# Kernel optimization log

Hardware: AMD Instinct MI355X
Metric: run time of the kernel (lower is better)

## Reference

```python
import jax, jax.numpy as jnp
import numpy as np

D, B, T, d = 4, 512, 64, 256  # num_dof, batch, seq_length, per-dof state dim


def setup_inputs() -> dict:
    key = jax.random.key(0)
    ks = jax.random.split(key, 17)
    w = lambda k, s: jax.random.normal(k, s, dtype=jnp.float32) * 0.05
    return {
        "x": jax.random.normal(ks[0], (D, B, T, d), dtype=jnp.float32),
        "wu": w(ks[1], (D, 2 * d, d)), "wf": w(ks[2], (D, 2 * d, d)),
        "wo": w(ks[3], (D, 2 * d, d)), "wc": w(ks[4], (D, 2 * d, d)),
        "bu": w(ks[5], (D, d)), "bf": w(ks[6], (D, d)),
        "bo": w(ks[7], (D, d)), "bc": w(ks[8], (D, d)),
        "gwu": w(ks[9], (D, D * d, d)), "gwf": w(ks[10], (D, D * d, d)),
        "gwo": w(ks[11], (D, D * d, d)), "gwc": w(ks[12], (D, D * d, d)),
        "gbu": w(ks[13], (D, d)), "gbf": w(ks[14], (D, d)),
        "gbo": w(ks[15], (D, d)), "gbc": w(ks[16], (D, d)),
    }


def reference(x, wu, wf, wo, wc, bu, bf, bo, bc,
              gwu, gwf, gwo, gwc, gbu, gbf, gbo, gbc):
    # x: [D, B, T, d]  (dof-stacked inputs_list)
    nD, nB, nT, nd = x.shape
    h0 = jnp.zeros((nD, nB, nd), x.dtype)
    m0 = jnp.zeros((nD, nB, nd), x.dtype)
    xt = jnp.transpose(x, (2, 0, 1, 3))  # [T, D, B, d]

    def step(carry, x_t):
        h, m = carry  # each [D, B, d]
        # --- per-dof LSTM cell (dofs independent here) ---
        inp = jnp.concatenate([x_t, h], axis=-1)  # [D, B, 2d]
        gu = jax.nn.sigmoid(jnp.einsum('dbi,dij->dbj', inp, wu) + bu[:, None, :])
        gf = jax.nn.sigmoid(jnp.einsum('dbi,dij->dbj', inp, wf) + bf[:, None, :])
        go = jax.nn.sigmoid(jnp.einsum('dbi,dij->dbj', inp, wo) + bo[:, None, :])
        gc = jnp.tanh(jnp.einsum('dbi,dij->dbj', inp, wc) + bc[:, None, :])
        m = gf * m + gu * gc
        h = jnp.tanh(go * m)
        # --- grid coupling step: hgrid = concat over dofs ---
        hg = jnp.transpose(h, (1, 0, 2)).reshape(nB, nD * nd)  # [B, D*d]
        gu2 = jax.nn.sigmoid(jnp.einsum('bs,dsj->dbj', hg, gwu) + gbu[:, None, :])
        gf2 = jax.nn.sigmoid(jnp.einsum('bs,dsj->dbj', hg, gwf) + gbf[:, None, :])
        go2 = jax.nn.sigmoid(jnp.einsum('bs,dsj->dbj', hg, gwo) + gbo[:, None, :])
        gc2 = jnp.tanh(jnp.einsum('bs,dsj->dbj', hg, gwc) + gbc[:, None, :])
        m = gf2 * m + gu2 * gc2
        h = jnp.tanh(go2 * m)
        return (h, m), None

    (h, m), _ = jax.lax.scan(step, (h0, m0), xt)
    # stacked [2, D, B, d]: [0]=h_list, [1]=m_list (dof along axis 1)
    return jnp.stack([h, m])
```

## Files before the change

kernel.cpp:

```cpp
#include <hip/hip_runtime.h>
#include <math.h>

#define NDOF 4
#define NB   512
#define NT   64
#define ND   256
#define NS   1024

#define GRID 256

typedef __attribute__((ext_vector_type(8))) __bf16 bf16x8;
typedef __attribute__((ext_vector_type(4))) float  f32x4;

__device__ __forceinline__ void gll16(const void* g, void* l) {
    __builtin_amdgcn_global_load_lds(
        (const __attribute__((address_space(1))) unsigned int*)g,
        (__attribute__((address_space(3))) unsigned int*)l, 16, 0, 0);
}

__device__ __forceinline__ float sig_(float x) { return 1.0f / (1.0f + __expf(-x)); }
__device__ __forceinline__ float tanh_(float x) {
    float e = __expf(-2.0f * fabsf(x));
    float t = (1.0f - e) / (1.0f + e);
    return copysignf(t, x);
}

__device__ __forceinline__ void store16_dev(__bf16* p, bf16x8 v) {
    asm volatile("global_store_dwordx4 %0, %1, off sc0 sc1" :: "v"(p), "v"(v) : "memory");
}

__device__ __forceinline__ void waitv0() {
    asm volatile("s_waitcnt vmcnt(0)" ::: "memory");
    __builtin_amdgcn_sched_barrier(0);
}
__device__ __forceinline__ void waitv8() {
    asm volatile("s_waitcnt vmcnt(8)" ::: "memory");
    __builtin_amdgcn_sched_barrier(0);
}
__device__ __forceinline__ void waitv12() {
    asm volatile("s_waitcnt vmcnt(12)" ::: "memory");
    __builtin_amdgcn_sched_barrier(0);
}

__device__ __forceinline__ void block_bar() {
    __builtin_amdgcn_sched_barrier(0);
    asm volatile("s_waitcnt lgkmcnt(0)\n\ts_barrier" ::: "memory");
    __builtin_amdgcn_sched_barrier(0);
}

__device__ __forceinline__ unsigned gen_load(const unsigned* p) {
    unsigned v;
    asm volatile("global_load_dword %0, %1, off sc0 sc1\n\ts_waitcnt vmcnt(0)"
                 : "=v"(v) : "v"(p) : "memory");
    return v;
}

struct __align__(64) Bar { unsigned cnt; unsigned gen; unsigned pad[14]; };

__device__ __forceinline__ void arrive_only(Bar* b, unsigned n, unsigned e) {
    unsigned prev = __hip_atomic_fetch_add(&b->cnt, 1u, __ATOMIC_RELAXED, __HIP_MEMORY_SCOPE_AGENT);
    if (prev == e * n - 1u)
        __hip_atomic_fetch_add(&b->gen, 1u, __ATOMIC_RELAXED, __HIP_MEMORY_SCOPE_AGENT);
}
__device__ __forceinline__ void poll_only(Bar* b, unsigned e) {
    unsigned spins = 0;
    while (gen_load(&b->gen) < e) {
        __builtin_amdgcn_s_sleep(1);
        if (++spins > (1u << 17)) break;
    }
}

struct Params {
    const __bf16* xbf;
    const __bf16* wT1;
    const __bf16* wT2;
    const float *b1u, *b1f, *b1o, *b1c;
    const float *b2u, *b2f, *b2o, *b2c;
    const __bf16* hInit;
    __bf16* ring;
    float*  out;
    Bar*    bars;
};

__device__ __forceinline__ void issueB(bf16x8* smem, const __bf16* wrow,
                                       int pair, int rot, int mask, int tid) {
    const int rowB = tid & 127;
    const int kgb  = (tid >> 7) & 1;
    const int bb = 2048 + (pair & 3) * 1024;
    const int k0 = ((pair + rot) & mask) * 64;
    #pragma unroll
    for (int i = 0; i < 4; ++i) {
        const int kg = kgb + 2 * i;
        gll16(wrow + k0 + kg * 8, &smem[bb + kg * 128 + rowB]);
    }
}
template<int XIT>
__device__ __forceinline__ void issueA(bf16x8* smem, const __bf16* ax,
                                       const __bf16* ah, int pair, int rot, int mask,
                                       int tid) {
    const int rowA = tid & 63;
    const int kga  = tid >> 6;
    const int bb = (pair & 3) * 512;
    const __bf16* base;
    if (XIT > 0 && pair < XIT) base = ax + (size_t)rowA * ND + pair * 64;
    else base = ah + (size_t)rowA * NS + (((pair + rot) & mask) * 64 - XIT * 64);
    #pragma unroll
    for (int i = 0; i < 2; ++i) {
        const int kg = kga + 4 * i;
        gll16(base + kg * 8, &smem[bb + kg * 64 + rowA]);
    }
}

template<int NIT, int XIT>
__device__ __forceinline__ void gemm_seg(bf16x8* smem,
    const __bf16* ax, const __bf16* ah, const __bf16* wrow, int rot,
    Bar* gateBar, unsigned gateE,
    f32x4 (&acc)[2][4], int lane, int wr, int ws, int tid)
{
    constexpr int NSEG = NIT / 2;
    #pragma unroll 1
    for (int s = 0; s < NSEG; ++s) {
        waitv0();
        block_bar();
        if (s == 1 && gateBar != nullptr) {
            if (tid == 0) poll_only(gateBar, gateE);
            block_bar();
        }
        if (s + 1 < NSEG) {
            issueB(smem, wrow, 2 * s + 2, rot, NIT - 1, tid);
            issueB(smem, wrow, 2 * s + 3, rot, NIT - 1, tid);
            issueA<XIT>(smem, ax, ah, 2 * s + 2, rot, NIT - 1, tid);
            issueA<XIT>(smem, ax, ah, 2 * s + 3, rot, NIT - 1, tid);
        }
        #pragma unroll
        for (int q = 0; q < 2; ++q) {
            const int bbA = ((2 * s + q) & 3) * 512;
            const int bbB = 2048 + ((2 * s + q) & 3) * 1024;
            #pragma unroll
            for (int sub = 0; sub < 2; ++sub) {
                const int kq = sub * 4 + (lane >> 4);
                bf16x8 a[2], b[4];
                #pragma unroll
                for (int mI = 0; mI < 2; ++mI)
                    a[mI] = smem[bbA + kq * 64 + wr + mI * 16 + (lane & 15)];
                #pragma unroll
                for (int g = 0; g < 4; ++g)
                    b[g] = smem[bbB + kq * 128 + g * 32 + ws * 16 + (lane & 15)];
                #pragma unroll
                for (int mI = 0; mI < 2; ++mI)
                    #pragma unroll
                    for (int g = 0; g < 4; ++g)
                        acc[mI][g] = __builtin_amdgcn_mfma_f32_16x16x32_bf16(a[mI], b[g], acc[mI][g], 0, 0, 0);
            }
        }
    }
}

__device__ __forceinline__ void epi_stage(const f32x4 (&acc)[2][4], float (&m_reg)[8],
    float bu, float bf_, float bo, float bc,
    char* stg, int wrL, int colq)
{
    #pragma unroll
    for (int mI = 0; mI < 2; ++mI) {
        #pragma unroll
        for (int r = 0; r < 4; ++r) {
            const int rowL = wrL + mI * 16 + r;
            const float gu = sig_(acc[mI][0][r] + bu);
            const float gf = sig_(acc[mI][1][r] + bf_);
            const float go = sig_(acc[mI][2][r] + bo);
            const float gc = tanh_(acc[mI][3][r] + bc);
            float& m = m_reg[mI * 4 + r];
            m = gf * m + gu * gc;
            ((__bf16*)(stg + rowL * 80))[colq] = (__bf16)tanh_(go * m);
        }
    }
}

__device__ __forceinline__ void flush_h(char* stg, __bf16* hbase, int r0,
                                        int scolBase, int tid)
{
    const int rowL = tid >> 2;
    const int off  = tid & 3;
    bf16x8 v = *(bf16x8*)(stg + rowL * 80 + off * 16);
    store16_dev(hbase + (size_t)(r0 + rowL) * NS + scolBase + off * 8, v);
}

__device__ __forceinline__ void epi_last(const f32x4 (&acc)[2][4], float (&m_reg)[8],
    float bu, float bf_, float bo, float bc,
    char* hs, char* ms, int wrL, int colq)
{
    #pragma unroll
    for (int mI = 0; mI < 2; ++mI) {
        #pragma unroll
        for (int r = 0; r < 4; ++r) {
            const int rowL = wrL + mI * 16 + r;
            const float gu = sig_(acc[mI][0][r] + bu);
            const float gf = sig_(acc[mI][1][r] + bf_);
            const float go = sig_(acc[mI][2][r] + bo);
            const float gc = tanh_(acc[mI][3][r] + bc);
            float& m = m_reg[mI * 4 + r];
            m = gf * m + gu * gc;
            ((float*)(hs + rowL * 144))[colq] = tanh_(go * m);
            ((float*)(ms + rowL * 144))[colq] = m;
        }
    }
}

__global__ __launch_bounds__(256, 1)
void lstm_persistent(Params p)
{
    __shared__ bf16x8 smem[6464];
    char* stg = (char*)&smem[6144];

    const int tid  = threadIdx.x;
    const int lane = tid & 63;
    const int wv   = tid >> 6;
    const int wr   = (wv >> 1) * 32;
    const int ws   = wv & 1;

    const int xcd   = blockIdx.x & 7;
    const int local = blockIdx.x >> 3;
    const int dof   = xcd & 3;
    const int rt    = (xcd >> 2) * 4 + (local >> 3);
    const int c0    = (local & 7) * 32;
    const int r0    = rt * 64;
    const int grp   = rt * 4 + dof;

    const int colq = ws * 16 + (lane & 15);
    const int scol = dof * ND + c0 + colq;
    const int scolBase = dof * ND + c0;
    const int wrL  = wr + (lane >> 4) * 4;

    const int rowB = tid & 127;
    const int npT  = dof * 1024 + (rowB >> 5) * 256 + c0 + (rowB & 31);
    const __bf16* wrow1 = p.wT1 + (size_t)npT * 512;
    const __bf16* wrow2 = p.wT2 + (size_t)npT * 1024;

    const float b1u = p.b1u[scol], b1f = p.b1f[scol], b1o = p.b1o[scol], b1c = p.b1c[scol];
    const float b2u = p.b2u[scol], b2f = p.b2f[scol], b2o = p.b2o[scol], b2c = p.b2c[scol];

    float m_reg[8];
    #pragma unroll
    for (int i = 0; i < 8; ++i) m_reg[i] = 0.f;

    Bar* bar32A = &p.bars[rt];
    Bar* bar8A  = &p.bars[8 + grp];
    Bar* bar8B  = &p.bars[40 + grp];
    const int rot2 = dof * 4;

    auto slot = [&](int i) -> __bf16* { return p.ring + ((size_t)i << 19); };

    {
        const __bf16* ax0 = p.xbf + ((size_t)(dof * NT) * NB + r0) * ND;
        issueB(smem, wrow1, 0, 0, 7, tid);
        issueB(smem, wrow1, 1, 0, 7, tid);
        issueA<4>(smem, ax0, nullptr, 0, 0, 7, tid);
        issueA<4>(smem, ax0, nullptr, 1, 0, 7, tid);
    }

    #pragma unroll 1
    for (int t = 0; t < NT; ++t) {
        const __bf16* ax  = p.xbf + ((size_t)(dof * NT + t) * NB + r0) * ND;
        const __bf16* ah1 = (t == 0 ? p.hInit : slot(2 * t - 1)) + (size_t)r0 * NS + dof * ND;
        __bf16* h1out = slot(2 * t);
        const __bf16* ah2 = slot(2 * t) + (size_t)r0 * NS;
        __bf16* h2out = slot(2 * t + 1);

        f32x4 acc[2][4];
        #pragma unroll
        for (int mI = 0; mI < 2; ++mI)
            #pragma unroll
            for (int g = 0; g < 4; ++g) acc[mI][g] = (f32x4){0.f, 0.f, 0.f, 0.f};

        gemm_seg<8, 4>(smem, ax, ah1, wrow1, 0, bar8B, (unsigned)t,
                       acc, lane, wr, ws, tid);

        epi_stage(acc, m_reg, b1u, b1f, b1o, b1c, stg, wrL, colq);
        block_bar();
        flush_h(stg, h1out, r0, scolBase, tid);
        issueB(smem, wrow2, 0, rot2, 15, tid);
        issueB(smem, wrow2, 1, rot2, 15, tid);
        waitv8();
        block_bar();
        if (tid == 0) {
            arrive_only(bar8A, 8, (unsigned)(t + 1));
            arrive_only(bar32A, 32, (unsigned)(t + 1));
            poll_only(bar8A, (unsigned)(t + 1));
        }
        block_bar();
        issueA<0>(smem, nullptr, ah2, 0, rot2, 15, tid);
        issueA<0>(smem, nullptr, ah2, 1, rot2, 15, tid);

        #pragma unroll
        for (int mI = 0; mI < 2; ++mI)
            #pragma unroll
            for (int g = 0; g < 4; ++g) acc[mI][g] = (f32x4){0.f, 0.f, 0.f, 0.f};

        gemm_seg<16, 0>(smem, nullptr, ah2, wrow2, rot2, bar32A, (unsigned)(t + 1),
                        acc, lane, wr, ws, tid);

        if (t + 1 < NT) {
            epi_stage(acc, m_reg, b2u, b2f, b2o, b2c, stg, wrL, colq);
            block_bar();
            flush_h(stg, h2out, r0, scolBase, tid);
            const __bf16* axn = p.xbf + ((size_t)(dof * NT + t + 1) * NB + r0) * ND;
            issueB(smem, wrow1, 0, 0, 7, tid);
            issueB(smem, wrow1, 1, 0, 7, tid);
            issueA<4>(smem, axn, nullptr, 0, 0, 7, tid);
            issueA<4>(smem, axn, nullptr, 1, 0, 7, tid);
            waitv12();
            block_bar();
            if (tid == 0) arrive_only(bar8B, 8, (unsigned)(t + 1));
        } else {
            block_bar();
            char* hs = (char*)smem;
            char* ms = (char*)smem + 9216;
            epi_last(acc, m_reg, b2u, b2f, b2o, b2c, hs, ms, wrL, colq);
            block_bar();
            #pragma unroll
            for (int k = 0; k < 2; ++k) {
                const int c = tid + 256 * k;
                const int rowL = c >> 3;
                const int off  = c & 7;
                const size_t gi = ((size_t)dof * NB + r0 + rowL) * ND + c0 + off * 4;
                *(f32x4*)(p.out + gi) = *(f32x4*)(hs + rowL * 144 + off * 16);
                *(f32x4*)(p.out + (size_t)NDOF * NB * ND + gi) = *(f32x4*)(ms + rowL * 144 + off * 16);
            }
        }
    }
}

__global__ __launch_bounds__(256)
void convert_x(const float* __restrict__ x, __bf16* __restrict__ xbf)
{
    const int id  = blockIdx.x * 256 + threadIdx.x;
    const int d0  = (id & 31) * 8;
    const int t   = (id >> 5) & 63;
    const int b   = (id >> 11) & 511;
    const int dof = id >> 20;
    const float* s = x + (((size_t)dof * NB + b) * NT + t) * ND + d0;
    const float4 v0 = *(const float4*)s;
    const float4 v1 = *(const float4*)(s + 4);
    bf16x8 o;
    o[0] = (__bf16)v0.x; o[1] = (__bf16)v0.y; o[2] = (__bf16)v0.z; o[3] = (__bf16)v0.w;
    o[4] = (__bf16)v1.x; o[5] = (__bf16)v1.y; o[6] = (__bf16)v1.z; o[7] = (__bf16)v1.w;
    *(bf16x8*)(xbf + (((size_t)dof * NT + t) * NB + b) * ND + d0) = o;
}

__global__ __launch_bounds__(256)
void transpose_weights(const float* __restrict__ wu, const float* __restrict__ wf,
                       const float* __restrict__ wo, const float* __restrict__ wcp,
                       const float* __restrict__ gwu, const float* __restrict__ gwf,
                       const float* __restrict__ gwo, const float* __restrict__ gwc,
                       __bf16* __restrict__ wT1, __bf16* __restrict__ wT2)
{
    int id = blockIdx.x * 256 + threadIdx.x;
    const int C1 = 4096 * 64;
    int K, np, kc;
    const float *s0, *s1, *s2, *s3;
    __bf16* dst;
    if (id < C1) { K = 512;  np = id & 4095; kc = id >> 12; dst = wT1; s0 = wu;  s1 = wf;  s2 = wo;  s3 = wcp; }
    else { id -= C1; K = 1024; np = id & 4095; kc = id >> 12; dst = wT2; s0 = gwu; s1 = gwf; s2 = gwo; s3 = gwc; }
    const int dof = np >> 10, q = np & 1023, g = q >> 8, col = q & 255;
    const float* w = ((g == 0) ? s0 : (g == 1) ? s1 : (g == 2) ? s2 : s3)
                     + ((size_t)dof * K + kc * 8) * ND + col;
    bf16x8 o;
    #pragma unroll
    for (int j = 0; j < 8; ++j) o[j] = (__bf16)w[j * ND];
    *(bf16x8*)(dst + (size_t)np * K + kc * 8) = o;
}

extern "C" void kernel_launch(void* const* d_in, const int* in_sizes, int n_in,
                              void* d_out, int out_size, void* d_ws, size_t ws_size,
                              hipStream_t stream)
{
    const float* x   = (const float*)d_in[0];
    const float* wu  = (const float*)d_in[1];
    const float* wf  = (const float*)d_in[2];
    const float* wo  = (const float*)d_in[3];
    const float* wc  = (const float*)d_in[4];

    char* ws = (char*)d_ws;
    __bf16* wT1  = (__bf16*)ws;
    __bf16* wT2  = (__bf16*)(ws + (4u  << 20));
    __bf16* xbf  = (__bf16*)(ws + (12u << 20));
    __bf16* hIn  = (__bf16*)(ws + (76u << 20));
    Bar*    bars = (Bar*)  (ws + (78u << 20));
    __bf16* ring = (__bf16*)(ws + (80u << 20));

    convert_x<<<16384, 256, 0, stream>>>(x, xbf);
    transpose_weights<<<3072, 256, 0, stream>>>(
        wu, wf, wo, wc,
        (const float*)d_in[9], (const float*)d_in[10],
        (const float*)d_in[11], (const float*)d_in[12], wT1, wT2);
    hipMemsetAsync(ws + (76u << 20), 0, (2u << 20) + 8192, stream);

    Params p;
    p.xbf = xbf; p.wT1 = wT1; p.wT2 = wT2;
    p.b1u = (const float*)d_in[5];  p.b1f = (const float*)d_in[6];
    p.b1o = (const float*)d_in[7];  p.b1c = (const float*)d_in[8];
    p.b2u = (const float*)d_in[13]; p.b2f = (const float*)d_in[14];
    p.b2o = (const float*)d_in[15]; p.b2c = (const float*)d_in[16];
    p.hInit = hIn; p.ring = ring; p.out = (float*)d_out; p.bars = bars;

    lstm_persistent<<<dim3(GRID), dim3(256), 0, stream>>>(p);
}
```

Measured before the change: 1.625 ms.

## Replace atomic counter barriers with per-block flag arrays polled by a wavefront

Swaps the atomic-increment counter/generation barriers for per-block monotonic flags. Each block writes its own timestep value with a plain system-coherent store, and one wavefront polls all peer flags in parallel, using lane-wise loads and a wave-wide all() check. This removes serialized atomic contention on shared counters and the extra generation bump from the critical path of each timestep. The trade-off is more load traffic per poll and a lower spin timeout, which could break out of a wait early under contention.

```diff
diff --git a/kernel.cpp b/kernel.cpp
--- a/kernel.cpp
+++ b/kernel.cpp
@@ -28,6 +28,15 @@
 __device__ __forceinline__ void store16_dev(__bf16* p, bf16x8 v) {
     asm volatile("global_store_dwordx4 %0, %1, off sc0 sc1" :: "v"(p), "v"(v) : "memory");
 }
+__device__ __forceinline__ void store_flag(unsigned* p, unsigned v) {
+    asm volatile("global_store_dword %0, %1, off sc0 sc1" :: "v"(p), "v"(v) : "memory");
+}
+__device__ __forceinline__ unsigned flag_load(const unsigned* p) {
+    unsigned v;
+    asm volatile("global_load_dword %0, %1, off sc0 sc1\n\ts_waitcnt vmcnt(0)"
+                 : "=v"(v) : "v"(p) : "memory");
+    return v;
+}
 
 __device__ __forceinline__ void waitv0() {
     asm volatile("s_waitcnt vmcnt(0)" ::: "memory");
@@ -48,25 +57,14 @@
     __builtin_amdgcn_sched_barrier(0);
 }
 
-__device__ __forceinline__ unsigned gen_load(const unsigned* p) {
-    unsigned v;
-    asm volatile("global_load_dword %0, %1, off sc0 sc1\n\ts_waitcnt vmcnt(0)"
-                 : "=v"(v) : "v"(p) : "memory");
-    return v;
-}
-
-struct __align__(64) Bar { unsigned cnt; unsigned gen; unsigned pad[14]; };
-
-__device__ __forceinline__ void arrive_only(Bar* b, unsigned n, unsigned e) {
-    unsigned prev = __hip_atomic_fetch_add(&b->cnt, 1u, __ATOMIC_RELAXED, __HIP_MEMORY_SCOPE_AGENT);
-    if (prev == e * n - 1u)
-        __hip_atomic_fetch_add(&b->gen, 1u, __ATOMIC_RELAXED, __HIP_MEMORY_SCOPE_AGENT);
-}
-__device__ __forceinline__ void poll_only(Bar* b, unsigned e) {
+__device__ __forceinline__ void poll_flags(const unsigned* f, int nf, unsigned e, int lane) {
     unsigned spins = 0;
-    while (gen_load(&b->gen) < e) {
+    for (;;) {
+        unsigned v = e;
+        if (lane < nf) v = flag_load(f + lane);
+        if (__all(v >= e)) break;
         __builtin_amdgcn_s_sleep(1);
-        if (++spins > (1u << 17)) break;
+        if (++spins > (1u << 15)) break;
     }
 }
 
@@ -79,7 +77,7 @@
     const __bf16* hInit;
     __bf16* ring;
     float*  out;
-    Bar*    bars;
+    unsigned* flags;
 };
 
 __device__ __forceinline__ void issueB(bf16x8* smem, const __bf16* wrow,
@@ -114,7 +112,7 @@
 template<int NIT, int XIT>
 __device__ __forceinline__ void gemm_seg(bf16x8* smem,
     const __bf16* ax, const __bf16* ah, const __bf16* wrow, int rot,
-    Bar* gateBar, unsigned gateE,
+    const unsigned* gateF, int gateN, unsigned gateE,
     f32x4 (&acc)[2][4], int lane, int wr, int ws, int tid)
 {
     constexpr int NSEG = NIT / 2;
@@ -122,8 +120,8 @@
     for (int s = 0; s < NSEG; ++s) {
         waitv0();
         block_bar();
-        if (s == 1 && gateBar != nullptr) {
-            if (tid == 0) poll_only(gateBar, gateE);
+        if (s == 1 && gateF != nullptr) {
+            if (tid < 64) poll_flags(gateF, gateN, gateE, lane);
             block_bar();
         }
         if (s + 1 < NSEG) {
@@ -222,7 +220,8 @@
     const int local = blockIdx.x >> 3;
     const int dof   = xcd & 3;
     const int rt    = (xcd >> 2) * 4 + (local >> 3);
-    const int c0    = (local & 7) * 32;
+    const int strip = local & 7;
+    const int c0    = strip * 32;
     const int r0    = rt * 64;
     const int grp   = rt * 4 + dof;
 
@@ -243,9 +242,11 @@
     #pragma unroll
     for (int i = 0; i < 8; ++i) m_reg[i] = 0.f;
 
-    Bar* bar32A = &p.bars[rt];
-    Bar* bar8A  = &p.bars[8 + grp];
-    Bar* bar8B  = &p.bars[40 + grp];
+    unsigned* fP1own = p.flags + grp * 8;
+    unsigned* fP1rt  = p.flags + rt * 32;
+    unsigned* fP2own = p.flags + 256 + grp * 8;
+    unsigned* myP1   = p.flags + grp * 8 + strip;
+    unsigned* myP2   = p.flags + 256 + grp * 8 + strip;
     const int rot2 = dof * 4;
 
     auto slot = [&](int i) -> __bf16* { return p.ring + ((size_t)i << 19); };
@@ -272,7 +273,7 @@
             #pragma unroll
             for (int g = 0; g < 4; ++g) acc[mI][g] = (f32x4){0.f, 0.f, 0.f, 0.f};
 
-        gemm_seg<8, 4>(smem, ax, ah1, wrow1, 0, bar8B, (unsigned)t,
+        gemm_seg<8, 4>(smem, ax, ah1, wrow1, 0, fP2own, 8, (unsigned)t,
                        acc, lane, wr, ws, tid);
 
         epi_stage(acc, m_reg, b1u, b1f, b1o, b1c, stg, wrL, colq);
@@ -282,11 +283,8 @@
         issueB(smem, wrow2, 1, rot2, 15, tid);
         waitv8();
         block_bar();
-        if (tid == 0) {
-            arrive_only(bar8A, 8, (unsigned)(t + 1));
-            arrive_only(bar32A, 32, (unsigned)(t + 1));
-            poll_only(bar8A, (unsigned)(t + 1));
-        }
+        if (tid == 0) store_flag(myP1, (unsigned)(t + 1));
+        if (tid < 64) poll_flags(fP1own, 8, (unsigned)(t + 1), lane);
         block_bar();
         issueA<0>(smem, nullptr, ah2, 0, rot2, 15, tid);
         issueA<0>(smem, nullptr, ah2, 1, rot2, 15, tid);
@@ -296,7 +294,7 @@
             #pragma unroll
             for (int g = 0; g < 4; ++g) acc[mI][g] = (f32x4){0.f, 0.f, 0.f, 0.f};
 
-        gemm_seg<16, 0>(smem, nullptr, ah2, wrow2, rot2, bar32A, (unsigned)(t + 1),
+        gemm_seg<16, 0>(smem, nullptr, ah2, wrow2, rot2, fP1rt, 32, (unsigned)(t + 1),
                         acc, lane, wr, ws, tid);
 
         if (t + 1 < NT) {
@@ -310,7 +308,7 @@
             issueA<4>(smem, axn, nullptr, 1, 0, 7, tid);
             waitv12();
             block_bar();
-            if (tid == 0) arrive_only(bar8B, 8, (unsigned)(t + 1));
+            if (tid == 0) store_flag(myP2, (unsigned)(t + 1));
         } else {
             block_bar();
             char* hs = (char*)smem;
@@ -385,7 +383,7 @@
     __bf16* wT2  = (__bf16*)(ws + (4u  << 20));
     __bf16* xbf  = (__bf16*)(ws + (12u << 20));
     __bf16* hIn  = (__bf16*)(ws + (76u << 20));
-    Bar*    bars = (Bar*)  (ws + (78u << 20));
+    unsigned* flags = (unsigned*)(ws + (78u << 20));
     __bf16* ring = (__bf16*)(ws + (80u << 20));
 
     convert_x<<<16384, 256, 0, stream>>>(x, xbf);
@@ -401,7 +399,7 @@
     p.b1o = (const float*)d_in[7];  p.b1c = (const float*)d_in[8];
     p.b2u = (const float*)d_in[13]; p.b2f = (const float*)d_in[14];
     p.b2o = (const float*)d_in[15]; p.b2c = (const float*)d_in[16];
-    p.hInit = hIn; p.ring = ring; p.out = (float*)d_out; p.bars = bars;
+    p.hInit = hIn; p.ring = ring; p.out = (float*)d_out; p.flags = flags;
 
     lstm_persistent<<<dim3(GRID), dim3(256), 0, stream>>>(p);
 }
```

Measured after the change: 1.568 ms. 1.04x faster.
